# Kernel optimization log

Hardware: AMD Instinct MI355X
Metric: run time of the kernel (lower is better)

Reference implementation:

```python
import jax, jax.numpy as jnp
import numpy as np

N_EMBD = 768
HEAD_SIZE = 64

def setup_inputs() -> dict:
    key = jax.random.key(0)
    ks = jax.random.split(key, 9)
    B, S = 8, 2048
    scale = 1.0 / np.sqrt(N_EMBD)
    return {
        "q": jax.random.normal(ks[0], (B, S, N_EMBD), jnp.float32),
        "k": jax.random.normal(ks[1], (B, S, N_EMBD), jnp.float32),
        "v": jax.random.normal(ks[2], (B, S, N_EMBD), jnp.float32),
        "Wq": jax.random.normal(ks[3], (N_EMBD, HEAD_SIZE), jnp.float32) * scale,
        "bq": jnp.zeros((HEAD_SIZE,), jnp.float32),
        "Wk": jax.random.normal(ks[4], (N_EMBD, HEAD_SIZE), jnp.float32) * scale,
        "bk": jnp.zeros((HEAD_SIZE,), jnp.float32),
        "Wv": jax.random.normal(ks[5], (N_EMBD, HEAD_SIZE), jnp.float32) * scale,
        "bv": jnp.zeros((HEAD_SIZE,), jnp.float32),
    }

def reference(q, k, v, Wq, bq, Wk, bk, Wv, bv):
    # NOTE: original scales by sqrt(C) where C = n_embd (input dim), not head_size.
    C = q.shape[-1]
    qi = q @ Wq + bq  # [B,S,H]
    ki = k @ Wk + bk
    vi = v @ Wv + bv
    att = jnp.einsum('bsh,bth->bst', qi, ki) / jnp.sqrt(jnp.float32(C))
    att = jax.nn.softmax(att, axis=-1)
    out = jnp.einsum('bst,bth->bsh', att, vi)
    return out
```

## Files before the change

### kernel.cpp

```cpp
#include <hip/hip_runtime.h>

#define Bn 8
#define Sn 2048
#define Cn 768
#define Hn 64
#define BS (Bn * Sn)

typedef __attribute__((ext_vector_type(8))) short bf16x8;
typedef __attribute__((ext_vector_type(4))) float f32x4;

__device__ __forceinline__ unsigned short f2bf(float x) {
  unsigned int u = __builtin_bit_cast(unsigned int, x);
  u += 0x7FFFu + ((u >> 16) & 1u);
  return (unsigned short)(u >> 16);
}

__device__ __forceinline__ void gload_lds16(const void* g, void* l) {
  __builtin_amdgcn_global_load_lds(
      (const __attribute__((address_space(1))) unsigned int*)g,
      (__attribute__((address_space(3))) unsigned int*)l, 16, 0, 0);
}

__global__ __launch_bounds__(256) void wconv(const float* __restrict__ Wq,
                                             const float* __restrict__ Wk,
                                             const float* __restrict__ Wv,
                                             unsigned short* __restrict__ Wt) {
  int idx = blockIdx.x * 256 + threadIdx.x;
  int mat = idx / (Cn * Hn);
  int rem = idx - mat * (Cn * Hn);
  int c = rem / Hn, h = rem - c * Hn;
  const float* W = (mat == 0) ? Wq : (mat == 1) ? Wk : Wv;
  Wt[mat * (Hn * Cn) + h * Cn + c] = f2bf(W[rem]);
}

__global__ __launch_bounds__(256) void proj(const float* __restrict__ q,
                                            const float* __restrict__ k,
                                            const float* __restrict__ v,
                                            const float* __restrict__ bq,
                                            const float* __restrict__ bk,
                                            const float* __restrict__ bv,
                                            const unsigned short* __restrict__ Wt,
                                            unsigned short* __restrict__ qi,
                                            unsigned short* __restrict__ ki,
                                            unsigned short* __restrict__ vi) {
  const int mat  = blockIdx.x >> 8;
  const int row0 = (blockIdx.x & 255) * 64;
  const float* X    = (mat == 0) ? q  : (mat == 1) ? k  : v;
  const float* bias = (mat == 0) ? bq : (mat == 1) ? bk : bv;
  unsigned short* Y = (mat == 0) ? qi : (mat == 1) ? ki : vi;
  const unsigned short* Wm = Wt + mat * (Hn * Cn);
  const float scale = (mat == 0) ? 0.03608439182435161f : 1.0f;

  __shared__ __align__(16) float          Xf[2][4096];
  __shared__ __align__(16) unsigned short Wl[2][4096];

  const int tid  = threadIdx.x;
  const int lane = tid & 63;
  const int w    = tid >> 6;
  const int col  = lane & 15;
  const int grp  = lane >> 4;

  const float* xsrc[4];
#pragma unroll
  for (int j = 0; j < 4; ++j) {
    int sidx = j * 256 + tid;
    int row  = sidx >> 4;
    int cf4  = (sidx & 15) ^ (row & 15);
    xsrc[j]  = X + (size_t)(row0 + row) * Cn + cf4 * 4;
  }
  const unsigned short* wsrc[2];
#pragma unroll
  for (int j = 0; j < 2; ++j) {
    int sidx = j * 256 + tid;
    int h    = sidx >> 3;
    int pd   = (sidx & 7) ^ (h & 7);
    wsrc[j]  = Wm + (size_t)h * Cn + pd * 8;
  }

#pragma unroll
  for (int j = 0; j < 4; ++j) gload_lds16(xsrc[j], &Xf[0][(j * 256 + w * 64) * 4]);
#pragma unroll
  for (int j = 0; j < 2; ++j) gload_lds16(wsrc[j], &Wl[0][(j * 256 + w * 64) * 8]);

  f32x4 acc[4] = {};
  const int rloc = w * 16 + col;

  for (int c = 0; c < 12; ++c) {
    const int buf = c & 1;
    __syncthreads();
    if (c < 11) {
      const int nb = buf ^ 1;
#pragma unroll
      for (int j = 0; j < 4; ++j)
        gload_lds16(xsrc[j] + (c + 1) * 64, &Xf[nb][(j * 256 + w * 64) * 4]);
#pragma unroll
      for (int j = 0; j < 2; ++j)
        gload_lds16(wsrc[j] + (c + 1) * 64, &Wl[nb][(j * 256 + w * 64) * 8]);
    }
#pragma unroll
    for (int ks = 0; ks < 2; ++ks) {
      const int cf0 = ks * 8 + grp * 2;
      float4 a0 = *(const float4*)&Xf[buf][(rloc * 16 + (cf0 ^ col)) * 4];
      float4 a1 = *(const float4*)&Xf[buf][(rloc * 16 + ((cf0 + 1) ^ col)) * 4];
      bf16x8 av;
      av[0] = (short)f2bf(a0.x); av[1] = (short)f2bf(a0.y);
      av[2] = (short)f2bf(a0.z); av[3] = (short)f2bf(a0.w);
      av[4] = (short)f2bf(a1.x); av[5] = (short)f2bf(a1.y);
      av[6] = (short)f2bf(a1.z); av[7] = (short)f2bf(a1.w);
      const int p = ks * 4 + grp;
#pragma unroll
      for (int nf = 0; nf < 4; ++nf) {
        int h = nf * 16 + col;
        bf16x8 bfr = *(const bf16x8*)&Wl[buf][(h * 8 + (p ^ (h & 7))) * 8];
        acc[nf] = __builtin_amdgcn_mfma_f32_16x16x32_bf16(av, bfr, acc[nf], 0, 0, 0);
      }
    }
  }

#pragma unroll
  for (int nf = 0; nf < 4; ++nf) {
    int h = nf * 16 + col;
    float bb = bias[h];
#pragma unroll
    for (int r2 = 0; r2 < 4; ++r2) {
      int row = row0 + w * 16 + grp * 4 + r2;
      Y[(size_t)row * Hn + h] = f2bf((acc[nf][r2] + bb) * scale);
    }
  }
}

template <int SPLIT>
__global__ __launch_bounds__(256) void attn(const unsigned short* __restrict__ qi,
                                            const unsigned short* __restrict__ ki,
                                            const unsigned short* __restrict__ vi,
                                            float* __restrict__ pacc,
                                            float* __restrict__ pm,
                                            float* __restrict__ pl,
                                            float* __restrict__ out,
                                            int tpb) {
  const int bq    = blockIdx.x & 255;
  const int split = blockIdx.x >> 8;
  const int b  = bq >> 5;
  const int s0 = (bq & 31) * 64;
  const int t0 = split * tpb;
  const unsigned short* Qb = qi + ((size_t)b * Sn + s0) * Hn;
  const unsigned short* Kb = ki + (size_t)b * Sn * Hn;
  const unsigned short* Vb = vi + (size_t)b * Sn * Hn;

  __shared__ __align__(16) unsigned char Ks[64 * 128];
  __shared__ __align__(16) unsigned char Vt[64 * 128];
  __shared__ __align__(16) unsigned char Ps[4 * 16 * 128];

  const int tid  = threadIdx.x;
  const int lane = tid & 63;
  const int w    = tid >> 6;
  const int col  = lane & 15;
  const int grp  = lane >> 4;

  bf16x8 qa[2];
#pragma unroll
  for (int ks2 = 0; ks2 < 2; ++ks2)
    qa[ks2] = *(const bf16x8*)(Qb + (size_t)(w * 16 + col) * Hn + ks2 * 32 + grp * 8);

  f32x4 acc[4] = {};
  float m[4], l[4];
#pragma unroll
  for (int r = 0; r < 4; ++r) { m[r] = -1e30f; l[r] = 0.0f; }

  for (int t = t0; t < t0 + tpb; ++t) {
    const unsigned short* Kt = Kb + t * 64 * Hn;
    const unsigned short* Vg = Vb + t * 64 * Hn;
    __syncthreads();
    {
      int kr = tid >> 2, p = tid & 3;
      const uint4* src = (const uint4*)(Kt + kr * Hn);
      uint4 a  = src[p * 2];
      uint4 b2 = src[p * 2 + 1];
      *(uint4*)(Ks + kr * 128 + ((p * 32) ^ ((kr & 7) << 4)))        = a;
      *(uint4*)(Ks + kr * 128 + (((p * 32) + 16) ^ ((kr & 7) << 4))) = b2;
    }
    {
      int kp = tid >> 3;
      int dg = tid & 7;
      uint4 v0 = *(const uint4*)(Vg + (2 * kp) * Hn + dg * 8);
      uint4 v1 = *(const uint4*)(Vg + (2 * kp + 1) * Hn + dg * 8);
      const unsigned short* a0 = (const unsigned short*)&v0;
      const unsigned short* a1 = (const unsigned short*)&v1;
#pragma unroll
      for (int j0 = 0; j0 < 8; ++j0) {
        int j = (j0 + dg) & 7;
        int d = dg * 8 + j;
        unsigned int pk = (unsigned int)a0[j] | ((unsigned int)a1[j] << 16);
        *(unsigned int*)(Vt + d * 128 + ((4 * kp) ^ ((d & 7) << 4))) = pk;
      }
    }
    __syncthreads();
    f32x4 sf[4] = {};
#pragma unroll
    for (int ks2 = 0; ks2 < 2; ++ks2) {
#pragma unroll
      for (int nf = 0; nf < 4; ++nf) {
        int kr = nf * 16 + col;
        bf16x8 bfr = *(const bf16x8*)(Ks + kr * 128 + ((ks2 * 64 + grp * 16) ^ ((kr & 7) << 4)));
        sf[nf] = __builtin_amdgcn_mfma_f32_16x16x32_bf16(qa[ks2], bfr, sf[nf], 0, 0, 0);
      }
    }
    float mn[4], fs[4];
#pragma unroll
    for (int r = 0; r < 4; ++r) {
      float mx = fmaxf(fmaxf(sf[0][r], sf[1][r]), fmaxf(sf[2][r], sf[3][r]));
#pragma unroll
      for (int off = 1; off < 16; off <<= 1)
        mx = fmaxf(mx, __shfl_xor(mx, off, 64));
      mn[r] = fmaxf(m[r], mx);
      fs[r] = __expf(m[r] - mn[r]);
      m[r]  = mn[r];
    }
#pragma unroll
    for (int nf = 0; nf < 4; ++nf)
#pragma unroll
      for (int r = 0; r < 4; ++r)
        sf[nf][r] = __expf(sf[nf][r] - mn[r]);
#pragma unroll
    for (int r = 0; r < 4; ++r) {
      float sm = sf[0][r] + sf[1][r] + sf[2][r] + sf[3][r];
#pragma unroll
      for (int off = 1; off < 16; off <<= 1)
        sm += __shfl_xor(sm, off, 64);
      l[r] = l[r] * fs[r] + sm;
    }
#pragma unroll
    for (int nf = 0; nf < 4; ++nf) {
#pragma unroll
      for (int r = 0; r < 4; ++r) {
        acc[nf][r] *= fs[r];
        int prow = grp * 4 + r;
        int key  = nf * 16 + col;
        *(unsigned short*)(Ps + w * 2048 + prow * 128 + ((key * 2) ^ ((prow & 7) << 4))) =
            f2bf(sf[nf][r]);
      }
    }
#pragma unroll
    for (int kk = 0; kk < 2; ++kk) {
      bf16x8 pa = *(const bf16x8*)(Ps + w * 2048 + col * 128 +
                                   ((kk * 64 + grp * 16) ^ ((col & 7) << 4)));
#pragma unroll
      for (int nf = 0; nf < 4; ++nf) {
        int dr = nf * 16 + col;
        bf16x8 bv = *(const bf16x8*)(Vt + dr * 128 + ((kk * 64 + grp * 16) ^ ((dr & 7) << 4)));
        acc[nf] = __builtin_amdgcn_mfma_f32_16x16x32_bf16(pa, bv, acc[nf], 0, 0, 0);
      }
    }
  }
  if (SPLIT) {
    const size_t sb = (size_t)split * BS + (size_t)b * Sn;
#pragma unroll
    for (int nf = 0; nf < 4; ++nf) {
#pragma unroll
      for (int r = 0; r < 4; ++r) {
        int row = s0 + w * 16 + grp * 4 + r;
        pacc[(sb + row) * Hn + nf * 16 + col] = acc[nf][r];
      }
    }
    if (col == 0) {
#pragma unroll
      for (int r = 0; r < 4; ++r) {
        int row = s0 + w * 16 + grp * 4 + r;
        pm[sb + row] = m[r];
        pl[sb + row] = l[r];
      }
    }
  } else {
#pragma unroll
    for (int nf = 0; nf < 4; ++nf) {
#pragma unroll
      for (int r = 0; r < 4; ++r) {
        int row = s0 + w * 16 + grp * 4 + r;
        out[((size_t)b * Sn + row) * Hn + nf * 16 + col] = acc[nf][r] / l[r];
      }
    }
  }
}

__global__ __launch_bounds__(256) void combine(const float* __restrict__ pacc,
                                               const float* __restrict__ pm,
                                               const float* __restrict__ pl,
                                               float* __restrict__ out,
                                               int nsplit) {
  int gid = blockIdx.x * 256 + threadIdx.x;
  int gr  = gid >> 4;
  int dq  = (gid & 15) * 4;
  float M = -1e30f;
  for (int s = 0; s < nsplit; ++s) M = fmaxf(M, pm[(size_t)s * BS + gr]);
  float L = 0.0f;
  float4 o = make_float4(0.f, 0.f, 0.f, 0.f);
  for (int s = 0; s < nsplit; ++s) {
    float wgt = __expf(pm[(size_t)s * BS + gr] - M);
    L += pl[(size_t)s * BS + gr] * wgt;
    float4 p = *(const float4*)(pacc + ((size_t)s * BS + gr) * Hn + dq);
    o.x += p.x * wgt; o.y += p.y * wgt; o.z += p.z * wgt; o.w += p.w * wgt;
  }
  float inv = 1.0f / L;
  float4 r = make_float4(o.x * inv, o.y * inv, o.z * inv, o.w * inv);
  *(float4*)(out + (size_t)gr * Hn + dq) = r;
}

extern "C" void kernel_launch(void* const* d_in, const int* in_sizes, int n_in,
                              void* d_out, int out_size, void* d_ws, size_t ws_size,
                              hipStream_t stream) {
  const float* q  = (const float*)d_in[0];
  const float* k  = (const float*)d_in[1];
  const float* v  = (const float*)d_in[2];
  const float* Wq = (const float*)d_in[3];
  const float* bq = (const float*)d_in[4];
  const float* Wk = (const float*)d_in[5];
  const float* bk = (const float*)d_in[6];
  const float* Wv = (const float*)d_in[7];
  const float* bv = (const float*)d_in[8];
  float* out = (float*)d_out;

  unsigned short* Wt = (unsigned short*)d_ws;
  unsigned short* qi = Wt + 3 * Hn * Cn;
  unsigned short* ki = qi + (size_t)BS * Hn;
  unsigned short* vi = ki + (size_t)BS * Hn;
  float* pacc = (float*)(vi + (size_t)BS * Hn);

  const size_t base_bytes = (size_t)(3 * Hn * Cn + 3 * (size_t)BS * Hn) * 2;
  const size_t avail = (ws_size > base_bytes) ? ws_size - base_bytes : 0;

  int nsplit = 4;
  while (nsplit > 1 &&
         (size_t)nsplit * ((size_t)BS * Hn * 4 + 2 * (size_t)BS * 4) > avail)
    nsplit >>= 1;
  bool direct = ((size_t)nsplit * ((size_t)BS * Hn * 4 + 2 * (size_t)BS * 4) > avail);

  float* pm = pacc + (size_t)nsplit * BS * Hn;
  float* pl = pm + (size_t)nsplit * BS;

  wconv<<<dim3((3 * Cn * Hn) / 256), dim3(256), 0, stream>>>(Wq, Wk, Wv, Wt);
  proj<<<dim3(768), dim3(256), 0, stream>>>(q, k, v, bq, bk, bv, Wt, qi, ki, vi);
  if (direct) {
    attn<0><<<dim3(256), dim3(256), 0, stream>>>(qi, ki, vi, nullptr, nullptr, nullptr, out, 32);
  } else {
    attn<1><<<dim3(256 * nsplit), dim3(256), 0, stream>>>(qi, ki, vi, pacc, pm, pl, nullptr,
                                                          32 / nsplit);
    combine<<<dim3(BS * 16 / 256), dim3(256), 0, stream>>>(pacc, pm, pl, out, nsplit);
  }
}
```

Before: 91.17 us.

## Load projection operands directly from global memory into registers, bypassing LDS

Replaces the LDS double-buffered global_load_lds staging in the projection kernel with direct per-lane global loads into register double buffers, removing the __syncthreads and shared-memory traffic. The fully unrolled loop prefetches the next K-chunk into registers while issuing MFMAs on the current one. In exchange, each wave fetches the weight tile independently (less reuse across waves), register pressure rises, and launch bounds now declare one block per CU as the minimum, which could reduce occupancy and latency hiding.

```diff
diff --git a/kernel.cpp b/kernel.cpp
--- a/kernel.cpp
+++ b/kernel.cpp
@@ -13,12 +13,6 @@
   unsigned int u = __builtin_bit_cast(unsigned int, x);
   u += 0x7FFFu + ((u >> 16) & 1u);
   return (unsigned short)(u >> 16);
-}
-
-__device__ __forceinline__ void gload_lds16(const void* g, void* l) {
-  __builtin_amdgcn_global_load_lds(
-      (const __attribute__((address_space(1))) unsigned int*)g,
-      (__attribute__((address_space(3))) unsigned int*)l, 16, 0, 0);
 }
 
 __global__ __launch_bounds__(256) void wconv(const float* __restrict__ Wq,
@@ -33,16 +27,16 @@
   Wt[mat * (Hn * Cn) + h * Cn + c] = f2bf(W[rem]);
 }
 
-__global__ __launch_bounds__(256) void proj(const float* __restrict__ q,
-                                            const float* __restrict__ k,
-                                            const float* __restrict__ v,
-                                            const float* __restrict__ bq,
-                                            const float* __restrict__ bk,
-                                            const float* __restrict__ bv,
-                                            const unsigned short* __restrict__ Wt,
-                                            unsigned short* __restrict__ qi,
-                                            unsigned short* __restrict__ ki,
-                                            unsigned short* __restrict__ vi) {
+__global__ __launch_bounds__(256, 1) void proj(const float* __restrict__ q,
+                                               const float* __restrict__ k,
+                                               const float* __restrict__ v,
+                                               const float* __restrict__ bq,
+                                               const float* __restrict__ bk,
+                                               const float* __restrict__ bv,
+                                               const unsigned short* __restrict__ Wt,
+                                               unsigned short* __restrict__ qi,
+                                               unsigned short* __restrict__ ki,
+                                               unsigned short* __restrict__ vi) {
   const int mat  = blockIdx.x >> 8;
   const int row0 = (blockIdx.x & 255) * 64;
   const float* X    = (mat == 0) ? q  : (mat == 1) ? k  : v;
@@ -51,69 +45,56 @@
   const unsigned short* Wm = Wt + mat * (Hn * Cn);
   const float scale = (mat == 0) ? 0.03608439182435161f : 1.0f;
 
-  __shared__ __align__(16) float          Xf[2][4096];
-  __shared__ __align__(16) unsigned short Wl[2][4096];
-
   const int tid  = threadIdx.x;
   const int lane = tid & 63;
   const int w    = tid >> 6;
   const int col  = lane & 15;
   const int grp  = lane >> 4;
 
-  const float* xsrc[4];
-#pragma unroll
-  for (int j = 0; j < 4; ++j) {
-    int sidx = j * 256 + tid;
-    int row  = sidx >> 4;
-    int cf4  = (sidx & 15) ^ (row & 15);
-    xsrc[j]  = X + (size_t)(row0 + row) * Cn + cf4 * 4;
-  }
-  const unsigned short* wsrc[2];
-#pragma unroll
-  for (int j = 0; j < 2; ++j) {
-    int sidx = j * 256 + tid;
-    int h    = sidx >> 3;
-    int pd   = (sidx & 7) ^ (h & 7);
-    wsrc[j]  = Wm + (size_t)h * Cn + pd * 8;
-  }
-
-#pragma unroll
-  for (int j = 0; j < 4; ++j) gload_lds16(xsrc[j], &Xf[0][(j * 256 + w * 64) * 4]);
-#pragma unroll
-  for (int j = 0; j < 2; ++j) gload_lds16(wsrc[j], &Wl[0][(j * 256 + w * 64) * 8]);
+  const float* Xr = X + (size_t)(row0 + w * 16 + col) * Cn + grp * 8;
+  const unsigned short* Wl = Wm + (size_t)col * Cn + grp * 8;
+
+  float4 xa[2][4];
+  bf16x8 wb[2][8];
+
+#pragma unroll
+  for (int ks = 0; ks < 2; ++ks) {
+    xa[0][ks * 2]     = *(const float4*)(Xr + ks * 32);
+    xa[0][ks * 2 + 1] = *(const float4*)(Xr + ks * 32 + 4);
+#pragma unroll
+    for (int nf = 0; nf < 4; ++nf)
+      wb[0][ks * 4 + nf] = *(const bf16x8*)(Wl + (size_t)(nf * 16) * Cn + ks * 32);
+  }
 
   f32x4 acc[4] = {};
-  const int rloc = w * 16 + col;
-
+
+#pragma unroll
   for (int c = 0; c < 12; ++c) {
-    const int buf = c & 1;
-    __syncthreads();
+    const int cur = c & 1;
+    const int nxt = cur ^ 1;
     if (c < 11) {
-      const int nb = buf ^ 1;
-#pragma unroll
-      for (int j = 0; j < 4; ++j)
-        gload_lds16(xsrc[j] + (c + 1) * 64, &Xf[nb][(j * 256 + w * 64) * 4]);
-#pragma unroll
-      for (int j = 0; j < 2; ++j)
-        gload_lds16(wsrc[j] + (c + 1) * 64, &Wl[nb][(j * 256 + w * 64) * 8]);
+#pragma unroll
+      for (int ks = 0; ks < 2; ++ks) {
+        xa[nxt][ks * 2]     = *(const float4*)(Xr + (c + 1) * 64 + ks * 32);
+        xa[nxt][ks * 2 + 1] = *(const float4*)(Xr + (c + 1) * 64 + ks * 32 + 4);
+#pragma unroll
+        for (int nf = 0; nf < 4; ++nf)
+          wb[nxt][ks * 4 + nf] =
+              *(const bf16x8*)(Wl + (size_t)(nf * 16) * Cn + (c + 1) * 64 + ks * 32);
+      }
     }
 #pragma unroll
     for (int ks = 0; ks < 2; ++ks) {
-      const int cf0 = ks * 8 + grp * 2;
-      float4 a0 = *(const float4*)&Xf[buf][(rloc * 16 + (cf0 ^ col)) * 4];
-      float4 a1 = *(const float4*)&Xf[buf][(rloc * 16 + ((cf0 + 1) ^ col)) * 4];
+      const float4 p0 = xa[cur][ks * 2], p1 = xa[cur][ks * 2 + 1];
       bf16x8 av;
-      av[0] = (short)f2bf(a0.x); av[1] = (short)f2bf(a0.y);
-      av[2] = (short)f2bf(a0.z); av[3] = (short)f2bf(a0.w);
-      av[4] = (short)f2bf(a1.x); av[5] = (short)f2bf(a1.y);
-      av[6] = (short)f2bf(a1.z); av[7] = (short)f2bf(a1.w);
-      const int p = ks * 4 + grp;
-#pragma unroll
-      for (int nf = 0; nf < 4; ++nf) {
-        int h = nf * 16 + col;
-        bf16x8 bfr = *(const bf16x8*)&Wl[buf][(h * 8 + (p ^ (h & 7))) * 8];
-        acc[nf] = __builtin_amdgcn_mfma_f32_16x16x32_bf16(av, bfr, acc[nf], 0, 0, 0);
-      }
+      av[0] = (short)f2bf(p0.x); av[1] = (short)f2bf(p0.y);
+      av[2] = (short)f2bf(p0.z); av[3] = (short)f2bf(p0.w);
+      av[4] = (short)f2bf(p1.x); av[5] = (short)f2bf(p1.y);
+      av[6] = (short)f2bf(p1.z); av[7] = (short)f2bf(p1.w);
+#pragma unroll
+      for (int nf = 0; nf < 4; ++nf)
+        acc[nf] = __builtin_amdgcn_mfma_f32_16x16x32_bf16(av, wb[cur][ks * 4 + nf], acc[nf],
+                                                          0, 0, 0);
     }
   }
 
```

Result: slower. 112.2 us (+23.0%).
